# Optimization experiments

Hardware: AMD Instinct MI355X
Metric: run time of the kernel (lower is better)

Reference implementation:

```python
import jax, jax.numpy as jnp
import numpy as np

N = 100000      # nodes
E = 1200000     # edges
D_IN = 7        # node feature dim
H = 64          # hidden_dim
G = 64          # graphs in batch
L = 2           # num_layers
EPS = 1e-5      # BatchNorm eps


def setup_inputs() -> dict:
    key = jax.random.key(0)
    ks = jax.random.split(key, 16)
    s = 1.0 / np.sqrt(H)
    return {
        "x": jax.random.normal(ks[0], (N, D_IN), jnp.float32),
        "edge_index": jax.random.randint(ks[1], (2, E), 0, N, dtype=jnp.int32),
        "batch": jnp.sort(jax.random.randint(ks[2], (N,), 0, G, dtype=jnp.int32)),
        "W_in": jax.random.normal(ks[3], (D_IN, H), jnp.float32) / np.sqrt(D_IN),
        "b_in": jax.random.normal(ks[4], (H,), jnp.float32) * 0.01,
        "conv_W": jax.random.normal(ks[5], (L, H, H), jnp.float32) * s,
        "conv_b": jax.random.normal(ks[6], (L, H), jnp.float32) * 0.01,
        "bn_gamma": jax.random.uniform(ks[7], (L, H), jnp.float32, 0.5, 1.5),
        "bn_beta": jax.random.normal(ks[8], (L, H), jnp.float32) * 0.1,
        "bn_mean": jax.random.normal(ks[9], (L, H), jnp.float32) * 0.1,
        "bn_var": jax.random.uniform(ks[10], (L, H), jnp.float32, 0.5, 1.5),
        "mlp_W1": jax.random.normal(ks[11], (H, H // 2), jnp.float32) * s,
        "mlp_b1": jax.random.normal(ks[12], (H // 2,), jnp.float32) * 0.01,
        "mlp_W2": jax.random.normal(ks[13], (H // 2, 1), jnp.float32) / np.sqrt(H // 2),
        "mlp_b2": jax.random.normal(ks[14], (1,), jnp.float32) * 0.01,
    }


def _gcn_conv(h, edge_index, W, b):
    # PyG GCNConv (eval): add self-loops, symmetric deg^{-1/2} normalization.
    n = h.shape[0]
    loops = jnp.arange(n, dtype=edge_index.dtype)
    src = jnp.concatenate([edge_index[0], loops])
    dst = jnp.concatenate([edge_index[1], loops])
    deg = jax.ops.segment_sum(jnp.ones_like(src, h.dtype), dst, num_segments=n)
    dinv = jnp.where(deg > 0, jax.lax.rsqrt(jnp.maximum(deg, 1.0)), 0.0)
    hw = h @ W                                  # [N, H]
    norm = (dinv[src] * dinv[dst])[:, None]     # [E+N, 1]
    msg = hw[src] * norm                        # gather + scale
    out = jax.ops.segment_sum(msg, dst, num_segments=n)  # scatter-add
    return out + b


def reference(x, edge_index, batch, W_in, b_in, conv_W, conv_b,
              bn_gamma, bn_beta, bn_mean, bn_var,
              mlp_W1, mlp_b1, mlp_W2, mlp_b2):
    # input projection (dropout is identity in eval mode)
    h = jax.nn.relu(x @ W_in + b_in)
    for i in range(L):
        hn = _gcn_conv(h, edge_index, conv_W[i], conv_b[i])
        # BatchNorm1d in inference mode with running stats
        hn = (hn - bn_mean[i]) * jax.lax.rsqrt(bn_var[i] + EPS) * bn_gamma[i] + bn_beta[i]
        hn = jax.nn.relu(hn)
        h = h + hn if i > 0 else hn
    # global_mean_pool over batch segment ids
    sums = jax.ops.segment_sum(h, batch, num_segments=G)        # [G, H]
    cnt = jax.ops.segment_sum(jnp.ones((h.shape[0],), h.dtype), batch, num_segments=G)
    pooled = sums / jnp.maximum(cnt, 1.0)[:, None]
    z = jax.nn.relu(pooled @ mlp_W1 + mlp_b1)
    return z @ mlp_W2 + mlp_b2                                  # [G, 1]
```

## Files before the change

### kernel.cpp

```cpp
#include <hip/hip_runtime.h>

#define NN 100000
#define NE 1200000
#define DIN 7
#define H 64
#define NG 64

#define NT 391
#define TILE 256
#define CAPT2 3712
#define PB 250
#define PCH (NE / PB)

typedef float v2f __attribute__((ext_vector_type(2)));

static __device__ __forceinline__ unsigned int pk_fp8(float a, float b, float c, float d) {
    int r = __builtin_amdgcn_cvt_pk_fp8_f32(a, b, 0, false);
    r = __builtin_amdgcn_cvt_pk_fp8_f32(c, d, r, true);
    return (unsigned int)r;
}

#define ZWORDS (NT + NG * H + NG)
__global__ __launch_bounds__(256) void k_zero(int* __restrict__ z) {
    int i = blockIdx.x * 256 + threadIdx.x;
    if (i < ZWORDS) z[i] = 0;
}

__global__ __launch_bounds__(256) void k_psort(const int* __restrict__ src, const int* __restrict__ dst,
                                               unsigned int* __restrict__ buck, int* __restrict__ tcur) {
    __shared__ unsigned int lbuf[PCH];
    __shared__ unsigned short tileof[PCH];
    __shared__ int hist[NT];
    __shared__ int lstart[NT];
    __shared__ int ldelta[NT];
    __shared__ int sc[256];
    int tid = threadIdx.x;
    int e0 = blockIdx.x * PCH;
    for (int i = tid; i < NT; i += 256) hist[i] = 0;
    __syncthreads();
    for (int i = tid; i < PCH; i += 256)
        atomicAdd(&hist[dst[e0 + i] >> 8], 1);
    __syncthreads();
    int h0 = (2 * tid < NT) ? hist[2 * tid] : 0;
    int h1 = (2 * tid + 1 < NT) ? hist[2 * tid + 1] : 0;
    int s = h0 + h1;
    sc[tid] = s; __syncthreads();
    for (int off = 1; off < 256; off <<= 1) {
        int y = (tid >= off) ? sc[tid - off] : 0;
        __syncthreads(); sc[tid] += y; __syncthreads();
    }
    int excl = sc[tid] - s;
    if (2 * tid < NT) lstart[2 * tid] = excl;
    if (2 * tid + 1 < NT) lstart[2 * tid + 1] = excl + h0;
    __syncthreads();
    for (int i = tid; i < NT; i += 256) hist[i] = lstart[i];
    __syncthreads();
    for (int i = tid; i < PCH; i += 256) {
        int d = dst[e0 + i], sv = src[e0 + i];
        int t = d >> 8;
        int pos = atomicAdd(&hist[t], 1);
        lbuf[pos] = ((unsigned)(d & 255) << 17) | (unsigned)sv;
        tileof[pos] = (unsigned short)t;
    }
    __syncthreads();
    for (int i = tid; i < NT; i += 256) {
        int n = hist[i] - lstart[i];
        int g = (n > 0) ? atomicAdd(&tcur[i], n) : 0;
        ldelta[i] = g - lstart[i];
    }
    __syncthreads();
    for (int i = tid; i < PCH; i += 256) {
        int t = tileof[i];
        int off = ldelta[t] + i;
        if (off < CAPT2) buck[(size_t)t * CAPT2 + off] = lbuf[i];
    }
}

__global__ __launch_bounds__(256) void k_tile_csr(const unsigned int* __restrict__ buck,
                                                  const int* __restrict__ tcur,
                                                  int* __restrict__ row_ptr, float* __restrict__ dinv,
                                                  int* __restrict__ col) {
    __shared__ int hist[TILE];
    __shared__ int lcur[TILE];
    __shared__ int sc[256];
    __shared__ int pref[NT + 1];
    __shared__ int colbuf[CAPT2];
    int t = blockIdx.x, tid = threadIdx.x;
    int t0 = (2 * tid < NT) ? tcur[2 * tid] : 0;
    int t1 = (2 * tid + 1 < NT) ? tcur[2 * tid + 1] : 0;
    int s2 = t0 + t1;
    sc[tid] = s2; __syncthreads();
    for (int off = 1; off < 256; off <<= 1) {
        int y = (tid >= off) ? sc[tid - off] : 0;
        __syncthreads(); sc[tid] += y; __syncthreads();
    }
    int ex2 = sc[tid] - s2;
    if (2 * tid < NT) pref[2 * tid] = ex2;
    if (2 * tid + 1 < NT) pref[2 * tid + 1] = ex2 + t0;
    __syncthreads();
    int gb = pref[t];
    int n = tcur[t];
    if (n > CAPT2) n = CAPT2;
    const unsigned int* b = buck + (size_t)t * CAPT2;
    hist[tid] = 0;
    __syncthreads();
    for (int i = tid; i < n; i += 256) atomicAdd(&hist[b[i] >> 17], 1);
    __syncthreads();
    int a = hist[tid];
    sc[tid] = a; __syncthreads();
    for (int off = 1; off < 256; off <<= 1) {
        int y = (tid >= off) ? sc[tid - off] : 0;
        __syncthreads(); sc[tid] += y; __syncthreads();
    }
    int excl = sc[tid] - a;
    int g0 = t * TILE + tid;
    if (g0 <= NN) row_ptr[g0] = gb + excl;
    if (g0 < NN) dinv[g0] = rsqrtf((float)(a + 1));
    lcur[tid] = excl;
    __syncthreads();
    for (int i = tid; i < n; i += 256) {
        unsigned int w = b[i];
        int p = atomicAdd(&lcur[w >> 17], 1);
        colbuf[p] = (int)(w & 0x1FFFFu);
    }
    __syncthreads();
    for (int i = tid; i < n; i += 256) col[gb + i] = colbuf[i];
}

__global__ __launch_bounds__(256) void k_gemm0_fused(const float* __restrict__ x,
                                                     const float* __restrict__ Win, const float* __restrict__ bin,
                                                     const float* __restrict__ W0, const float* __restrict__ dinv,
                                                     unsigned int* __restrict__ hws8) {
    __shared__ float xs[64][8];
    __shared__ float wsin[DIN * 64];
    __shared__ float bs[64];
    __shared__ __align__(16) float As[64][68];
    __shared__ __align__(16) float Wc[64][64];
    int tid = threadIdx.x;
    int r0 = blockIdx.x * 64;

    for (int idx = tid; idx < 64 * DIN; idx += 256) {
        int r = idx / DIN, k = idx - r * DIN;
        int gr = r0 + r;
        xs[r][k] = (gr < NN) ? x[gr * DIN + k] : 0.f;
    }
    for (int idx = tid; idx < DIN * 64; idx += 256) wsin[idx] = Win[idx];
    if (tid < 64) bs[tid] = bin[tid];
    for (int idx = tid; idx < 64 * 64; idx += 256) Wc[idx >> 6][idx & 63] = W0[idx];
    __syncthreads();

    {
        int r = tid >> 2, q = tid & 3;
        float xr[DIN];
#pragma unroll
        for (int k = 0; k < DIN; k++) xr[k] = xs[r][k];
#pragma unroll
        for (int cc = 0; cc < 16; cc++) {
            int c = q * 16 + cc;
            float a = bs[c];
#pragma unroll
            for (int k = 0; k < DIN; k++) a += xr[k] * wsin[k * 64 + c];
            As[c][r] = fmaxf(a, 0.f);
        }
    }
    __syncthreads();

    int tr = tid >> 4, tc = tid & 15;
    float acc[4][4] = {};
#pragma unroll 4
    for (int kk = 0; kk < 64; kk++) {
        float a0 = As[kk][tr * 4 + 0], a1 = As[kk][tr * 4 + 1];
        float a2 = As[kk][tr * 4 + 2], a3 = As[kk][tr * 4 + 3];
        float4 bv = *(const float4*)&Wc[kk][tc * 4];
        acc[0][0] += a0 * bv.x; acc[0][1] += a0 * bv.y; acc[0][2] += a0 * bv.z; acc[0][3] += a0 * bv.w;
        acc[1][0] += a1 * bv.x; acc[1][1] += a1 * bv.y; acc[1][2] += a1 * bv.z; acc[1][3] += a1 * bv.w;
        acc[2][0] += a2 * bv.x; acc[2][1] += a2 * bv.y; acc[2][2] += a2 * bv.z; acc[2][3] += a2 * bv.w;
        acc[3][0] += a3 * bv.x; acc[3][1] += a3 * bv.y; acc[3][2] += a3 * bv.z; acc[3][3] += a3 * bv.w;
    }
#pragma unroll
    for (int i = 0; i < 4; i++) {
        int gr = r0 + tr * 4 + i;
        if (gr < NN) {
            float s = dinv[gr];
            hws8[gr * 16 + tc] = pk_fp8(acc[i][0] * s, acc[i][1] * s, acc[i][2] * s, acc[i][3] * s);
        }
    }
}

__global__ __launch_bounds__(256) void k_gemm_scale(const float* __restrict__ A, const float* __restrict__ W,
                                                    const float* __restrict__ dinv,
                                                    unsigned int* __restrict__ hws8) {
    __shared__ __align__(16) float As[64][68];
    __shared__ __align__(16) float Ws[64][64];
    int tid = threadIdx.x;
    int r0 = blockIdx.x * 64;
    int row = tid >> 2, q = tid & 3;
    int gr0 = r0 + row;
#pragma unroll
    for (int j = 0; j < 4; j++) {
        int c = q * 16 + j * 4;
        float4 av = make_float4(0.f, 0.f, 0.f, 0.f);
        if (gr0 < NN) av = *(const float4*)(A + gr0 * H + c);
        As[c + 0][row] = av.x; As[c + 1][row] = av.y;
        As[c + 2][row] = av.z; As[c + 3][row] = av.w;
        *(float4*)&Ws[row][c] = *(const float4*)(W + row * H + c);
    }
    __syncthreads();

    int tr = tid >> 4, tc = tid & 15;
    float acc[4][4] = {};
#pragma unroll 4
    for (int kk = 0; kk < 64; kk++) {
        float a0 = As[kk][tr * 4 + 0], a1 = As[kk][tr * 4 + 1];
        float a2 = As[kk][tr * 4 + 2], a3 = As[kk][tr * 4 + 3];
        float4 bv = *(const float4*)&Ws[kk][tc * 4];
        acc[0][0] += a0 * bv.x; acc[0][1] += a0 * bv.y; acc[0][2] += a0 * bv.z; acc[0][3] += a0 * bv.w;
        acc[1][0] += a1 * bv.x; acc[1][1] += a1 * bv.y; acc[1][2] += a1 * bv.z; acc[1][3] += a1 * bv.w;
        acc[2][0] += a2 * bv.x; acc[2][1] += a2 * bv.y; acc[2][2] += a2 * bv.z; acc[2][3] += a2 * bv.w;
        acc[3][0] += a3 * bv.x; acc[3][1] += a3 * bv.y; acc[3][2] += a3 * bv.z; acc[3][3] += a3 * bv.w;
    }
#pragma unroll
    for (int i = 0; i < 4; i++) {
        int gr = r0 + tr * 4 + i;
        if (gr < NN) {
            float s = dinv[gr];
            hws8[gr * 16 + tc] = pk_fp8(acc[i][0] * s, acc[i][1] * s, acc[i][2] * s, acc[i][3] * s);
        }
    }
}

__global__ __launch_bounds__(256) void k_agg(const unsigned int* __restrict__ hws8,
                                             const int* __restrict__ row_ptr,
                                             const int* __restrict__ col, const float* __restrict__ dinv,
                                             const float* __restrict__ cb, const float* __restrict__ gamma,
                                             const float* __restrict__ beta, const float* __restrict__ mean,
                                             const float* __restrict__ var, float* __restrict__ h, int layer) {
    int tid = threadIdx.x;
    int sub = tid & 7;
    int v = blockIdx.x * 32 + (tid >> 3);
    const uint2* rb = (const uint2*)hws8;

    uint2 w = rb[v * 8 + sub];
    v2f p0 = __builtin_amdgcn_cvt_pk_f32_fp8((int)w.x, false);
    v2f p1 = __builtin_amdgcn_cvt_pk_f32_fp8((int)w.x, true);
    v2f p2 = __builtin_amdgcn_cvt_pk_f32_fp8((int)w.y, false);
    v2f p3 = __builtin_amdgcn_cvt_pk_f32_fp8((int)w.y, true);
    float a0 = p0.x, a1 = p0.y, a2 = p1.x, a3 = p1.y;
    float a4 = p2.x, a5 = p2.y, a6 = p3.x, a7 = p3.y;

    int s = row_ptr[v], e = row_ptr[v + 1];
    int i = s;
    int u0, u1, u2, u3;
    bool have = (i + 4 <= e);
    if (have) { u0 = col[i]; u1 = col[i + 1]; u2 = col[i + 2]; u3 = col[i + 3]; }
    while (have) {
        uint2 w0 = rb[u0 * 8 + sub];
        uint2 w1 = rb[u1 * 8 + sub];
        uint2 w2 = rb[u2 * 8 + sub];
        uint2 w3 = rb[u3 * 8 + sub];
        i += 4;
        have = (i + 4 <= e);
        if (have) { u0 = col[i]; u1 = col[i + 1]; u2 = col[i + 2]; u3 = col[i + 3]; }
#pragma unroll
        for (int k = 0; k < 4; k++) {
            uint2 wk = (k == 0) ? w0 : (k == 1) ? w1 : (k == 2) ? w2 : w3;
            v2f q0 = __builtin_amdgcn_cvt_pk_f32_fp8((int)wk.x, false);
            v2f q1 = __builtin_amdgcn_cvt_pk_f32_fp8((int)wk.x, true);
            v2f q2 = __builtin_amdgcn_cvt_pk_f32_fp8((int)wk.y, false);
            v2f q3 = __builtin_amdgcn_cvt_pk_f32_fp8((int)wk.y, true);
            a0 += q0.x; a1 += q0.y; a2 += q1.x; a3 += q1.y;
            a4 += q2.x; a5 += q2.y; a6 += q3.x; a7 += q3.y;
        }
    }
    for (; i < e; ++i) {
        uint2 wu = rb[col[i] * 8 + sub];
        v2f q0 = __builtin_amdgcn_cvt_pk_f32_fp8((int)wu.x, false);
        v2f q1 = __builtin_amdgcn_cvt_pk_f32_fp8((int)wu.x, true);
        v2f q2 = __builtin_amdgcn_cvt_pk_f32_fp8((int)wu.y, false);
        v2f q3 = __builtin_amdgcn_cvt_pk_f32_fp8((int)wu.y, true);
        a0 += q0.x; a1 += q0.y; a2 += q1.x; a3 += q1.y;
        a4 += q2.x; a5 += q2.y; a6 += q3.x; a7 += q3.y;
    }

    float dv = dinv[v];
    int f0 = sub * 8;
    float4 cb0 = *(const float4*)(cb + f0),    cb1 = *(const float4*)(cb + f0 + 4);
    float4 mn0 = *(const float4*)(mean + f0),  mn1 = *(const float4*)(mean + f0 + 4);
    float4 vr0 = *(const float4*)(var + f0),   vr1 = *(const float4*)(var + f0 + 4);
    float4 gm0 = *(const float4*)(gamma + f0), gm1 = *(const float4*)(gamma + f0 + 4);
    float4 bt0 = *(const float4*)(beta + f0),  bt1 = *(const float4*)(beta + f0 + 4);

    float r0 = (a0 * dv + cb0.x - mn0.x) * rsqrtf(vr0.x + 1e-5f) * gm0.x + bt0.x;
    float r1 = (a1 * dv + cb0.y - mn0.y) * rsqrtf(vr0.y + 1e-5f) * gm0.y + bt0.y;
    float r2 = (a2 * dv + cb0.z - mn0.z) * rsqrtf(vr0.z + 1e-5f) * gm0.z + bt0.z;
    float r3 = (a3 * dv + cb0.w - mn0.w) * rsqrtf(vr0.w + 1e-5f) * gm0.w + bt0.w;
    float r4 = (a4 * dv + cb1.x - mn1.x) * rsqrtf(vr1.x + 1e-5f) * gm1.x + bt1.x;
    float r5 = (a5 * dv + cb1.y - mn1.y) * rsqrtf(vr1.y + 1e-5f) * gm1.y + bt1.y;
    float r6 = (a6 * dv + cb1.z - mn1.z) * rsqrtf(vr1.z + 1e-5f) * gm1.z + bt1.z;
    float r7 = (a7 * dv + cb1.w - mn1.w) * rsqrtf(vr1.w + 1e-5f) * gm1.w + bt1.w;
    r0 = fmaxf(r0, 0.f); r1 = fmaxf(r1, 0.f); r2 = fmaxf(r2, 0.f); r3 = fmaxf(r3, 0.f);
    r4 = fmaxf(r4, 0.f); r5 = fmaxf(r5, 0.f); r6 = fmaxf(r6, 0.f); r7 = fmaxf(r7, 0.f);
    if (layer) {
        float4 hp0 = *(const float4*)(h + v * H + f0);
        float4 hp1 = *(const float4*)(h + v * H + f0 + 4);
        r0 += hp0.x; r1 += hp0.y; r2 += hp0.z; r3 += hp0.w;
        r4 += hp1.x; r5 += hp1.y; r6 += hp1.z; r7 += hp1.w;
    }
    *(float4*)(h + v * H + f0) = make_float4(r0, r1, r2, r3);
    *(float4*)(h + v * H + f0 + 4) = make_float4(r4, r5, r6, r7);
}

#define POOL_CHUNK 32
__global__ __launch_bounds__(64) void k_pool(const float* __restrict__ h, const int* __restrict__ batch,
                                             float* __restrict__ sums, float* __restrict__ cntg) {
    int lane = threadIdx.x;
    int start = blockIdx.x * POOL_CHUNK;
    int end = start + POOL_CHUNK; if (end > NN) end = NN;
    float acc = 0.f, c = 0.f;
    int curg = batch[start];
    for (int n = start; n < end; ++n) {
        int g = batch[n];
        if (g != curg) {
            atomicAdd(&sums[curg * H + lane], acc);
            if (lane == 0) atomicAdd(&cntg[curg], c);
            acc = 0.f; c = 0.f; curg = g;
        }
        acc += h[n * H + lane];
        c += 1.f;
    }
    atomicAdd(&sums[curg * H + lane], acc);
    if (lane == 0) atomicAdd(&cntg[curg], c);
}

__global__ __launch_bounds__(64) void k_mlp(const float* __restrict__ sums, const float* __restrict__ cntg,
                                            const float* __restrict__ W1, const float* __restrict__ b1,
                                            const float* __restrict__ W2, const float* __restrict__ b2,
                                            float* __restrict__ out) {
    int g = threadIdx.x;
    float inv = 1.f / fmaxf(cntg[g], 1.f);
    float pooled[H];
#pragma unroll
    for (int k = 0; k < H; k++) pooled[k] = sums[g * H + k] * inv;
    float o = b2[0];
#pragma unroll
    for (int j = 0; j < H / 2; j++) {
        float z = b1[j];
#pragma unroll
        for (int k = 0; k < H; k++) z += pooled[k] * W1[k * (H / 2) + j];
        o += fmaxf(z, 0.f) * W2[j];
    }
    out[g] = o;
}

extern "C" void kernel_launch(void* const* d_in, const int* in_sizes, int n_in,
                              void* d_out, int out_size, void* d_ws, size_t ws_size,
                              hipStream_t stream) {
    const float* x     = (const float*)d_in[0];
    const int*   ei    = (const int*)d_in[1];
    const int*   batch = (const int*)d_in[2];
    const float* Win   = (const float*)d_in[3];
    const float* bin   = (const float*)d_in[4];
    const float* convW = (const float*)d_in[5];
    const float* convb = (const float*)d_in[6];
    const float* gamma = (const float*)d_in[7];
    const float* beta  = (const float*)d_in[8];
    const float* mean  = (const float*)d_in[9];
    const float* var   = (const float*)d_in[10];
    const float* W1    = (const float*)d_in[11];
    const float* b1    = (const float*)d_in[12];
    const float* W2    = (const float*)d_in[13];
    const float* b2    = (const float*)d_in[14];
    float* out = (float*)d_out;

    char* p = (char*)d_ws;
    auto alloc = [&](size_t bytes) -> void* {
        void* r = (void*)p;
        p += (bytes + 255) & ~(size_t)255;
        return r;
    };
    float*          h       = (float*)alloc((size_t)NN * H * 4);
    unsigned int*   hws8    = (unsigned int*)alloc((size_t)NN * 16 * 4);
    float*          dinv    = (float*)alloc((size_t)NN * 4);
    int*            row_ptr = (int*)alloc((size_t)(NN + 1) * 4);
    int*            col     = (int*)alloc((size_t)NE * 4);
    unsigned int*   buck    = (unsigned int*)alloc((size_t)NT * CAPT2 * 4);
    int*            zbase   = (int*)alloc((size_t)ZWORDS * 4);
    int*            tcur    = zbase;
    float*          sums    = (float*)(zbase + NT);
    float*          cntg    = (float*)(zbase + NT + NG * H);

    const int* src  = ei;
    const int* dstp = ei + NE;

    k_zero<<<(ZWORDS + 255) / 256, 256, 0, stream>>>(zbase);

    k_psort<<<PB, 256, 0, stream>>>(src, dstp, buck, tcur);
    k_tile_csr<<<NT, 256, 0, stream>>>(buck, tcur, row_ptr, dinv, col);

    k_gemm0_fused<<<(NN + 63) / 64, 256, 0, stream>>>(x, Win, bin, convW, dinv, hws8);
    k_agg<<<NN / 32, 256, 0, stream>>>(hws8, row_ptr, col, dinv,
                                       convb, gamma, beta, mean, var, h, 0);
    k_gemm_scale<<<(NN + 63) / 64, 256, 0, stream>>>(h, convW + H * H, dinv, hws8);
    k_agg<<<NN / 32, 256, 0, stream>>>(hws8, row_ptr, col, dinv,
                                       convb + H, gamma + H, beta + H,
                                       mean + H, var + H, h, 1);

    k_pool<<<(NN + POOL_CHUNK - 1) / POOL_CHUNK, 64, 0, stream>>>(h, batch, sums, cntg);
    k_mlp<<<1, 64, 0, stream>>>(sums, cntg, W1, b1, W2, b2, out);
}
```

Before: 168.2 us.

## Fuse layer-0 aggregation with layer-1 GEMM into one kernel

Merges the first aggregation (gather, BN, ReLU) with the following 64x64 GEMM and dinv scaling, so the block stages the freshly computed rows in shared memory instead of re-reading h from global memory. A second fp8 buffer is added so the GEMM output does not overwrite the input that other blocks are still gathering from. The cost is one fewer kernel launch and no reread of h. In exchange each block now gathers 64 nodes in two sequential halves, which gives less parallelism per block during the latency-bound gather and adds shared-memory pressure.

```diff
diff --git a/kernel.cpp b/kernel.cpp
--- a/kernel.cpp
+++ b/kernel.cpp
@@ -18,6 +18,64 @@
     int r = __builtin_amdgcn_cvt_pk_fp8_f32(a, b, 0, false);
     r = __builtin_amdgcn_cvt_pk_fp8_f32(c, d, r, true);
     return (unsigned int)r;
+}
+
+static __device__ __forceinline__ void gather_node(const uint2* __restrict__ rb,
+                                                   const int* __restrict__ row_ptr,
+                                                   const int* __restrict__ col,
+                                                   int v, int sub, float* a) {
+    uint2 w = rb[v * 8 + sub];
+    v2f p0 = __builtin_amdgcn_cvt_pk_f32_fp8((int)w.x, false);
+    v2f p1 = __builtin_amdgcn_cvt_pk_f32_fp8((int)w.x, true);
+    v2f p2 = __builtin_amdgcn_cvt_pk_f32_fp8((int)w.y, false);
+    v2f p3 = __builtin_amdgcn_cvt_pk_f32_fp8((int)w.y, true);
+    a[0] = p0.x; a[1] = p0.y; a[2] = p1.x; a[3] = p1.y;
+    a[4] = p2.x; a[5] = p2.y; a[6] = p3.x; a[7] = p3.y;
+    int s = row_ptr[v], e = row_ptr[v + 1];
+    int i = s;
+    int u0, u1, u2, u3;
+    bool have = (i + 4 <= e);
+    if (have) { u0 = col[i]; u1 = col[i + 1]; u2 = col[i + 2]; u3 = col[i + 3]; }
+    while (have) {
+        uint2 w0 = rb[u0 * 8 + sub];
+        uint2 w1 = rb[u1 * 8 + sub];
+        uint2 w2 = rb[u2 * 8 + sub];
+        uint2 w3 = rb[u3 * 8 + sub];
+        i += 4;
+        have = (i + 4 <= e);
+        if (have) { u0 = col[i]; u1 = col[i + 1]; u2 = col[i + 2]; u3 = col[i + 3]; }
+#pragma unroll
+        for (int k = 0; k < 4; k++) {
+            uint2 wk = (k == 0) ? w0 : (k == 1) ? w1 : (k == 2) ? w2 : w3;
+            v2f q0 = __builtin_amdgcn_cvt_pk_f32_fp8((int)wk.x, false);
+            v2f q1 = __builtin_amdgcn_cvt_pk_f32_fp8((int)wk.x, true);
+            v2f q2 = __builtin_amdgcn_cvt_pk_f32_fp8((int)wk.y, false);
+            v2f q3 = __builtin_amdgcn_cvt_pk_f32_fp8((int)wk.y, true);
+            a[0] += q0.x; a[1] += q0.y; a[2] += q1.x; a[3] += q1.y;
+            a[4] += q2.x; a[5] += q2.y; a[6] += q3.x; a[7] += q3.y;
+        }
+    }
+    for (; i < e; ++i) {
+        uint2 wu = rb[col[i] * 8 + sub];
+        v2f q0 = __builtin_amdgcn_cvt_pk_f32_fp8((int)wu.x, false);
+        v2f q1 = __builtin_amdgcn_cvt_pk_f32_fp8((int)wu.x, true);
+        v2f q2 = __builtin_amdgcn_cvt_pk_f32_fp8((int)wu.y, false);
+        v2f q3 = __builtin_amdgcn_cvt_pk_f32_fp8((int)wu.y, true);
+        a[0] += q0.x; a[1] += q0.y; a[2] += q1.x; a[3] += q1.y;
+        a[4] += q2.x; a[5] += q2.y; a[6] += q3.x; a[7] += q3.y;
+    }
+}
+
+static __device__ __forceinline__ void bn_relu8(const float* a, float dv, int f0,
+                                                const float* __restrict__ cb, const float* __restrict__ gamma,
+                                                const float* __restrict__ beta, const float* __restrict__ mean,
+                                                const float* __restrict__ var, float* r) {
+#pragma unroll
+    for (int j = 0; j < 8; j++) {
+        int f = f0 + j;
+        float vv = (a[j] * dv + cb[f] - mean[f]) * rsqrtf(var[f] + 1e-5f) * gamma[f] + beta[f];
+        r[j] = fmaxf(vv, 0.f);
+    }
 }
 
 #define ZWORDS (NT + NG * H + NG)
@@ -187,23 +245,48 @@
     }
 }
 
-__global__ __launch_bounds__(256) void k_gemm_scale(const float* __restrict__ A, const float* __restrict__ W,
-                                                    const float* __restrict__ dinv,
-                                                    unsigned int* __restrict__ hws8) {
+__global__ __launch_bounds__(256) void k_agg_gemm(const unsigned int* __restrict__ hws8,
+                                                  const int* __restrict__ row_ptr,
+                                                  const int* __restrict__ col, const float* __restrict__ dinv,
+                                                  const float* __restrict__ cb, const float* __restrict__ gamma,
+                                                  const float* __restrict__ beta, const float* __restrict__ mean,
+                                                  const float* __restrict__ var,
+                                                  const float* __restrict__ W,
+                                                  float* __restrict__ h,
+                                                  unsigned int* __restrict__ hws8o) {
     __shared__ __align__(16) float As[64][68];
     __shared__ __align__(16) float Ws[64][64];
     int tid = threadIdx.x;
     int r0 = blockIdx.x * 64;
-    int row = tid >> 2, q = tid & 3;
-    int gr0 = r0 + row;
-#pragma unroll
-    for (int j = 0; j < 4; j++) {
-        int c = q * 16 + j * 4;
-        float4 av = make_float4(0.f, 0.f, 0.f, 0.f);
-        if (gr0 < NN) av = *(const float4*)(A + gr0 * H + c);
-        As[c + 0][row] = av.x; As[c + 1][row] = av.y;
-        As[c + 2][row] = av.z; As[c + 3][row] = av.w;
-        *(float4*)&Ws[row][c] = *(const float4*)(W + row * H + c);
+    const uint2* rb = (const uint2*)hws8;
+
+    {
+        int row = tid >> 2, q = tid & 3;
+#pragma unroll
+        for (int j = 0; j < 4; j++) {
+            int c = q * 16 + j * 4;
+            *(float4*)&Ws[row][c] = *(const float4*)(W + row * H + c);
+        }
+    }
+
+    int sub = tid & 7;
+#pragma unroll
+    for (int half = 0; half < 2; ++half) {
+        int lr = half * 32 + (tid >> 3);
+        int v = r0 + lr;
+        if (v < NN) {
+            float a[8], rr[8];
+            gather_node(rb, row_ptr, col, v, sub, a);
+            int f0 = sub * 8;
+            bn_relu8(a, dinv[v], f0, cb, gamma, beta, mean, var, rr);
+            *(float4*)(h + v * H + f0) = make_float4(rr[0], rr[1], rr[2], rr[3]);
+            *(float4*)(h + v * H + f0 + 4) = make_float4(rr[4], rr[5], rr[6], rr[7]);
+#pragma unroll
+            for (int j = 0; j < 8; j++) As[f0 + j][lr] = rr[j];
+        } else {
+#pragma unroll
+            for (int j = 0; j < 8; j++) As[sub * 8 + j][lr] = 0.f;
+        }
     }
     __syncthreads();
 
@@ -224,7 +307,7 @@
         int gr = r0 + tr * 4 + i;
         if (gr < NN) {
             float s = dinv[gr];
-            hws8[gr * 16 + tc] = pk_fp8(acc[i][0] * s, acc[i][1] * s, acc[i][2] * s, acc[i][3] * s);
+            hws8o[gr * 16 + tc] = pk_fp8(acc[i][0] * s, acc[i][1] * s, acc[i][2] * s, acc[i][3] * s);
         }
     }
 }
@@ -234,80 +317,20 @@
                                              const int* __restrict__ col, const float* __restrict__ dinv,
                                              const float* __restrict__ cb, const float* __restrict__ gamma,
                                              const float* __restrict__ beta, const float* __restrict__ mean,
-                                             const float* __restrict__ var, float* __restrict__ h, int layer) {
+                                             const float* __restrict__ var, float* __restrict__ h) {
     int tid = threadIdx.x;
     int sub = tid & 7;
     int v = blockIdx.x * 32 + (tid >> 3);
     const uint2* rb = (const uint2*)hws8;
 
-    uint2 w = rb[v * 8 + sub];
-    v2f p0 = __builtin_amdgcn_cvt_pk_f32_fp8((int)w.x, false);
-    v2f p1 = __builtin_amdgcn_cvt_pk_f32_fp8((int)w.x, true);
-    v2f p2 = __builtin_amdgcn_cvt_pk_f32_fp8((int)w.y, false);
-    v2f p3 = __builtin_amdgcn_cvt_pk_f32_fp8((int)w.y, true);
-    float a0 = p0.x, a1 = p0.y, a2 = p1.x, a3 = p1.y;
-    float a4 = p2.x, a5 = p2.y, a6 = p3.x, a7 = p3.y;
-
-    int s = row_ptr[v], e = row_ptr[v + 1];
-    int i = s;
-    int u0, u1, u2, u3;
-    bool have = (i + 4 <= e);
-    if (have) { u0 = col[i]; u1 = col[i + 1]; u2 = col[i + 2]; u3 = col[i + 3]; }
-    while (have) {
-        uint2 w0 = rb[u0 * 8 + sub];
-        uint2 w1 = rb[u1 * 8 + sub];
-        uint2 w2 = rb[u2 * 8 + sub];
-        uint2 w3 = rb[u3 * 8 + sub];
-        i += 4;
-        have = (i + 4 <= e);
-        if (have) { u0 = col[i]; u1 = col[i + 1]; u2 = col[i + 2]; u3 = col[i + 3]; }
-#pragma unroll
-        for (int k = 0; k < 4; k++) {
-            uint2 wk = (k == 0) ? w0 : (k == 1) ? w1 : (k == 2) ? w2 : w3;
-            v2f q0 = __builtin_amdgcn_cvt_pk_f32_fp8((int)wk.x, false);
-            v2f q1 = __builtin_amdgcn_cvt_pk_f32_fp8((int)wk.x, true);
-            v2f q2 = __builtin_amdgcn_cvt_pk_f32_fp8((int)wk.y, false);
-            v2f q3 = __builtin_amdgcn_cvt_pk_f32_fp8((int)wk.y, true);
-            a0 += q0.x; a1 += q0.y; a2 += q1.x; a3 += q1.y;
-            a4 += q2.x; a5 += q2.y; a6 += q3.x; a7 += q3.y;
-        }
-    }
-    for (; i < e; ++i) {
-        uint2 wu = rb[col[i] * 8 + sub];
-        v2f q0 = __builtin_amdgcn_cvt_pk_f32_fp8((int)wu.x, false);
-        v2f q1 = __builtin_amdgcn_cvt_pk_f32_fp8((int)wu.x, true);
-        v2f q2 = __builtin_amdgcn_cvt_pk_f32_fp8((int)wu.y, false);
-        v2f q3 = __builtin_amdgcn_cvt_pk_f32_fp8((int)wu.y, true);
-        a0 += q0.x; a1 += q0.y; a2 += q1.x; a3 += q1.y;
-        a4 += q2.x; a5 += q2.y; a6 += q3.x; a7 += q3.y;
-    }
-
-    float dv = dinv[v];
+    float a[8], rr[8];
+    gather_node(rb, row_ptr, col, v, sub, a);
     int f0 = sub * 8;
-    float4 cb0 = *(const float4*)(cb + f0),    cb1 = *(const float4*)(cb + f0 + 4);
-    float4 mn0 = *(const float4*)(mean + f0),  mn1 = *(const float4*)(mean + f0 + 4);
-    float4 vr0 = *(const float4*)(var + f0),   vr1 = *(const float4*)(var + f0 + 4);
-    float4 gm0 = *(const float4*)(gamma + f0), gm1 = *(const float4*)(gamma + f0 + 4);
-    float4 bt0 = *(const float4*)(beta + f0),  bt1 = *(const float4*)(beta + f0 + 4);
-
-    float r0 = (a0 * dv + cb0.x - mn0.x) * rsqrtf(vr0.x + 1e-5f) * gm0.x + bt0.x;
-    float r1 = (a1 * dv + cb0.y - mn0.y) * rsqrtf(vr0.y + 1e-5f) * gm0.y + bt0.y;
-    float r2 = (a2 * dv + cb0.z - mn0.z) * rsqrtf(vr0.z + 1e-5f) * gm0.z + bt0.z;
-    float r3 = (a3 * dv + cb0.w - mn0.w) * rsqrtf(vr0.w + 1e-5f) * gm0.w + bt0.w;
-    float r4 = (a4 * dv + cb1.x - mn1.x) * rsqrtf(vr1.x + 1e-5f) * gm1.x + bt1.x;
-    float r5 = (a5 * dv + cb1.y - mn1.y) * rsqrtf(vr1.y + 1e-5f) * gm1.y + bt1.y;
-    float r6 = (a6 * dv + cb1.z - mn1.z) * rsqrtf(vr1.z + 1e-5f) * gm1.z + bt1.z;
-    float r7 = (a7 * dv + cb1.w - mn1.w) * rsqrtf(vr1.w + 1e-5f) * gm1.w + bt1.w;
-    r0 = fmaxf(r0, 0.f); r1 = fmaxf(r1, 0.f); r2 = fmaxf(r2, 0.f); r3 = fmaxf(r3, 0.f);
-    r4 = fmaxf(r4, 0.f); r5 = fmaxf(r5, 0.f); r6 = fmaxf(r6, 0.f); r7 = fmaxf(r7, 0.f);
-    if (layer) {
-        float4 hp0 = *(const float4*)(h + v * H + f0);
-        float4 hp1 = *(const float4*)(h + v * H + f0 + 4);
-        r0 += hp0.x; r1 += hp0.y; r2 += hp0.z; r3 += hp0.w;
-        r4 += hp1.x; r5 += hp1.y; r6 += hp1.z; r7 += hp1.w;
-    }
-    *(float4*)(h + v * H + f0) = make_float4(r0, r1, r2, r3);
-    *(float4*)(h + v * H + f0 + 4) = make_float4(r4, r5, r6, r7);
+    bn_relu8(a, dinv[v], f0, cb, gamma, beta, mean, var, rr);
+    float4 hp0 = *(const float4*)(h + v * H + f0);
+    float4 hp1 = *(const float4*)(h + v * H + f0 + 4);
+    *(float4*)(h + v * H + f0) = make_float4(rr[0] + hp0.x, rr[1] + hp0.y, rr[2] + hp0.z, rr[3] + hp0.w);
+    *(float4*)(h + v * H + f0 + 4) = make_float4(rr[4] + hp1.x, rr[5] + hp1.y, rr[6] + hp1.z, rr[7] + hp1.w);
 }
 
 #define POOL_CHUNK 32
@@ -380,6 +403,7 @@
     };
     float*          h       = (float*)alloc((size_t)NN * H * 4);
     unsigned int*   hws8    = (unsigned int*)alloc((size_t)NN * 16 * 4);
+    unsigned int*   hws8b   = (unsigned int*)alloc((size_t)NN * 16 * 4);
     float*          dinv    = (float*)alloc((size_t)NN * 4);
     int*            row_ptr = (int*)alloc((size_t)(NN + 1) * 4);
     int*            col     = (int*)alloc((size_t)NE * 4);
@@ -398,12 +422,12 @@
     k_tile_csr<<<NT, 256, 0, stream>>>(buck, tcur, row_ptr, dinv, col);
 
     k_gemm0_fused<<<(NN + 63) / 64, 256, 0, stream>>>(x, Win, bin, convW, dinv, hws8);
-    k_agg<<<NN / 32, 256, 0, stream>>>(hws8, row_ptr, col, dinv,
-                                       convb, gamma, beta, mean, var, h, 0);
-    k_gemm_scale<<<(NN + 63) / 64, 256, 0, stream>>>(h, convW + H * H, dinv, hws8);
-    k_agg<<<NN / 32, 256, 0, stream>>>(hws8, row_ptr, col, dinv,
+    k_agg_gemm<<<(NN + 63) / 64, 256, 0, stream>>>(hws8, row_ptr, col, dinv,
+                                                   convb, gamma, beta, mean, var,
+                                                   convW + H * H, h, hws8b);
+    k_agg<<<NN / 32, 256, 0, stream>>>(hws8b, row_ptr, col, dinv,
                                        convb + H, gamma + H, beta + H,
-                                       mean + H, var + H, h, 1);
+                                       mean + H, var + H, h);
 
     k_pool<<<(NN + POOL_CHUNK - 1) / POOL_CHUNK, 64, 0, stream>>>(h, batch, sums, cntg);
     k_mlp<<<1, 64, 0, stream>>>(sums, cntg, W1, b1, W2, b2, out);
```

Result: no change. 165.0 us (-1.9%).
